# Performance work log

Hardware: AMD Instinct MI355X
Metric: run time of the kernel (lower is better)

The kernel has to match this reference:

```python
import jax, jax.numpy as jnp
import numpy as np

DIM = 1280
HEADS = 16
HEAD_DIM = DIM // HEADS  # 80
N_CHUNKS = 8
CHUNK = 1024
TOTAL = N_CHUNKS * CHUNK  # 8192 packed tokens


def rotate_half(x):
    x1, x2 = jnp.split(x, 2, axis=-1)
    return jnp.concatenate([-x2, x1], axis=-1)


def setup_inputs() -> dict:
    key = jax.random.key(0)
    k0, k1, k2 = jax.random.split(key, 3)
    hidden_states = jax.random.normal(k0, (TOTAL, DIM), dtype=jnp.float32)
    # 2D-rope style per-token angles, duplicated halves (standard vision RoPE layout)
    inv_freq = 1.0 / (10000.0 ** (jnp.arange(0, HEAD_DIM, 2, dtype=jnp.float32) / HEAD_DIM))
    pos = jnp.arange(TOTAL, dtype=jnp.float32)
    freqs = pos[:, None] * inv_freq[None, :]            # [T, HEAD_DIM//2]
    emb = jnp.concatenate([freqs, freqs], axis=-1)      # [T, HEAD_DIM]
    cos = jnp.cos(emb)
    sin = jnp.sin(emb)
    qkv_w = jax.random.normal(k1, (3 * DIM, DIM), dtype=jnp.float32) * 0.02
    qkv_b = jnp.zeros((3 * DIM,), dtype=jnp.float32)
    proj_w = jax.random.normal(k2, (DIM, DIM), dtype=jnp.float32) * 0.02
    proj_b = jnp.zeros((DIM,), dtype=jnp.float32)
    cu_seqlens = (jnp.arange(N_CHUNKS + 1, dtype=jnp.int32) * CHUNK)
    return {"hidden_states": hidden_states, "cos": cos, "sin": sin,
            "qkv_w": qkv_w, "qkv_b": qkv_b, "proj_w": proj_w, "proj_b": proj_b,
            "cu_seqlens": cu_seqlens}


def reference(hidden_states, cos, sin, qkv_w, qkv_b, proj_w, proj_b, cu_seqlens):
    # Equal-length chunks (cu_seqlens uniform): vectorize the Python chunk loop
    # as a leading batch axis n over chunks of length L.
    n = cu_seqlens.shape[0] - 1
    total, dim = hidden_states.shape
    L = total // n
    scaling = HEAD_DIM ** -0.5

    x = hidden_states.reshape(n, L, dim)
    qkv = x @ qkv_w.T + qkv_b                              # [n, L, 3*dim]
    qkv = qkv.reshape(n, L, 3, HEADS, HEAD_DIM)
    q, k, v = qkv[:, :, 0], qkv[:, :, 1], qkv[:, :, 2]     # [n, L, H, hd]

    # inline RoPE in fp32 (matches apply_rotary_pos_emb_vision)
    c = cos.reshape(n, L, 1, HEAD_DIM).astype(jnp.float32)
    s = sin.reshape(n, L, 1, HEAD_DIM).astype(jnp.float32)
    qf = q.astype(jnp.float32)
    kf = k.astype(jnp.float32)
    q = (qf * c + rotate_half(qf) * s).astype(q.dtype)
    k = (kf * c + rotate_half(kf) * s).astype(k.dtype)

    # naive per-chunk full attention: QK^T, fp32 softmax, PV
    scores = jnp.einsum('nlhd,nmhd->nhlm', q, k) * scaling  # [n, H, L, L]
    probs = jax.nn.softmax(scores.astype(jnp.float32), axis=-1).astype(q.dtype)
    out = jnp.einsum('nhlm,nmhd->nlhd', probs, v)           # [n, L, H, hd]
    out = out.reshape(n, L, dim)
    out = out @ proj_w.T + proj_b                           # [n, L, dim]
    return out.reshape(total, dim)
```

## Files before the change

### kernel.cpp

```cpp
#include <hip/hip_runtime.h>
#include <stdint.h>

#define DIM 1280
#define HEADS 16
#define HD 80
#define TOTAL 8192
#define CHUNK 1024
#define QKVN 3840

typedef __attribute__((ext_vector_type(8))) __bf16 bf16x8;
typedef __attribute__((ext_vector_type(4))) float floatx4;

typedef __attribute__((address_space(1))) const uint32_t gu32;
typedef __attribute__((address_space(3))) uint32_t lu32;

__device__ __forceinline__ void llds16(const void* g, void* l) {
  __builtin_amdgcn_global_load_lds((gu32*)g, (lu32*)l, 16, 0, 0);
}

__device__ __forceinline__ unsigned short f2b(float f) {
  union { __bf16 b; unsigned short u; } x; x.b = (__bf16)f; return x.u;
}
__device__ __forceinline__ float b2f(unsigned short u) {
  union { __bf16 b; unsigned short u; } x; x.u = u; return (float)x.b;
}
__device__ __forceinline__ float fexp2(float x) {
#if __has_builtin(__builtin_amdgcn_exp2f)
  return __builtin_amdgcn_exp2f(x);
#else
  return __expf(x * 0.6931471805599453f);
#endif
}

#define QSCALE (0.11180339887498949f * 1.44269504088896340f)

#define QROW 96
#define KT_SH (64 * 104)
#define VT_SH (80 * 72)

__global__ void cvt_bf16(const float* __restrict__ src, unsigned short* __restrict__ dst, int n4) {
  int i = blockIdx.x * 256 + threadIdx.x;
  if (i >= n4) return;
  float4 v = reinterpret_cast<const float4*>(src)[i];
  ushort4 o;
  o.x = f2b(v.x); o.y = f2b(v.y); o.z = f2b(v.z); o.w = f2b(v.w);
  reinterpret_cast<ushort4*>(dst)[i] = o;
}


__device__ __forceinline__ void stage_a64(const unsigned short* __restrict__ G,
                                          unsigned short* ls, int wv, int lane,
                                          int row0, int kk, int hi) {
#pragma unroll
  for (int t = 0; t < 2; ++t) {
    const int stripe = t * 8 + wv;
    const int rb = ((stripe >> 3) << 7) + ((stripe & 7) << 3) + hi;
    const int r = rb + (lane >> 3);
    const int ch = (lane & 7) ^ (r & 7);
    llds16(G + (size_t)(row0 + r) * DIM + kk + (ch << 3), ls + rb * 64);
  }
}

__device__ __forceinline__ void stage_b64(const unsigned short* __restrict__ G,
                                          unsigned short* ls, int wv, int lane,
                                          int row0, int kk, int hi) {
#pragma unroll
  for (int t = 0; t < 2; ++t) {
    const int stripe = t * 8 + wv;
    const int rb = ((stripe >> 2) << 6) + ((stripe & 3) << 3) + hi;
    const int r = rb + (lane >> 3);
    const int ch = (lane & 7) ^ (r & 7);
    llds16(G + (size_t)(row0 + r) * DIM + kk + (ch << 3), ls + rb * 64);
  }
}

__device__ __forceinline__ bf16x8 frg(const unsigned short* ls, int r, int cx) {
  return *reinterpret_cast<const bf16x8*>(ls + r * 64 + (cx << 3));
}

#define MFMA_BF16 __builtin_amdgcn_mfma_f32_16x16x32_bf16
#define LGKM0() asm volatile("s_waitcnt lgkmcnt(0)" ::: "memory")
#define BARR()  asm volatile("s_barrier" ::: "memory")

template<int MODE>
__launch_bounds__(512, 2)
__global__ void gemm8(const unsigned short* __restrict__ A,
                      const unsigned short* __restrict__ B,
                      const float* __restrict__ bias,
                      unsigned short* __restrict__ qo,
                      unsigned short* __restrict__ ko,
                      unsigned short* __restrict__ vo,
                      float* __restrict__ fo) {
  __shared__ __attribute__((aligned(16))) unsigned short lsA[2][256 * 64];
  __shared__ __attribute__((aligned(16))) unsigned short lsB[2][256 * 64];
  const int m0 = blockIdx.x * 256;
  const int n0 = blockIdx.y * 256;
  const int tid = threadIdx.x;
  const int wv = tid >> 6, lane = tid & 63;
  const int wr = wv >> 2, wc = wv & 3;
  const int q4 = lane >> 4, l15 = lane & 15;
  const int sx = l15 & 7;
  const int cx0 = q4 ^ sx;
  const int cx1 = (4 + q4) ^ sx;

  stage_a64(A, &lsA[0][0], wv, lane, m0, 0, 0);
  stage_b64(B, &lsB[0][0], wv, lane, n0, 0, 0);
  stage_b64(B, &lsB[0][0], wv, lane, n0, 0, 32);
  stage_a64(A, &lsA[0][0], wv, lane, m0, 0, 64);
  stage_b64(B, &lsB[1][0], wv, lane, n0, 64, 0);
  stage_a64(A, &lsA[1][0], wv, lane, m0, 64, 0);
  stage_b64(B, &lsB[1][0], wv, lane, n0, 64, 32);

  floatx4 acc[8][4];
#pragma unroll
  for (int i = 0; i < 8; ++i)
#pragma unroll
    for (int j = 0; j < 4; ++j)
      acc[i][j] = (floatx4){0.f, 0.f, 0.f, 0.f};

  asm volatile("s_waitcnt vmcnt(6)" ::: "memory");
  BARR();

  const int rA = wr * 128 + l15;
  const int rB = wc * 64 + l15;

  bf16x8 ArLo[4][2], ArHi[4][2], Blo[2][2], Bhi[2][2];

#pragma unroll 2
  for (int kt = 0; kt < 20; ++kt) {
    const unsigned short* la = &lsA[kt & 1][0];
    const unsigned short* lb = &lsB[kt & 1][0];
    unsigned short* aN = &lsA[(kt & 1) ^ 1][0];
    unsigned short* aC = &lsA[kt & 1][0];
    unsigned short* bC = &lsB[kt & 1][0];
    const bool st1 = (kt + 1 < 20);
    const bool st2 = (kt + 2 < 20);

    if (kt > 0) {
#pragma unroll
      for (int m = 0; m < 4; ++m)
#pragma unroll
        for (int n = 0; n < 2; ++n) {
          acc[m + 4][n] = MFMA_BF16(ArHi[m][0], Blo[n][0], acc[m + 4][n], 0, 0, 0);
          acc[m + 4][n] = MFMA_BF16(ArHi[m][1], Blo[n][1], acc[m + 4][n], 0, 0, 0);
        }
    }
#pragma unroll
    for (int m = 0; m < 4; ++m) {
      ArLo[m][0] = frg(la, rA + m * 16, cx0);
      ArLo[m][1] = frg(la, rA + m * 16, cx1);
    }
#pragma unroll
    for (int n = 0; n < 2; ++n) {
      Blo[n][0] = frg(lb, rB + n * 16, cx0);
      Blo[n][1] = frg(lb, rB + n * 16, cx1);
    }
    if (st1) stage_a64(A, aN, wv, lane, m0, (kt + 1) * 64, 64);
    LGKM0();
    BARR();

#pragma unroll
    for (int m = 0; m < 4; ++m)
#pragma unroll
      for (int n = 0; n < 2; ++n) {
        acc[m][n] = MFMA_BF16(ArLo[m][0], Blo[n][0], acc[m][n], 0, 0, 0);
        acc[m][n] = MFMA_BF16(ArLo[m][1], Blo[n][1], acc[m][n], 0, 0, 0);
      }
#pragma unroll
    for (int n = 0; n < 2; ++n) {
      Bhi[n][0] = frg(lb, rB + (n + 2) * 16, cx0);
      Bhi[n][1] = frg(lb, rB + (n + 2) * 16, cx1);
    }
    if (st2) stage_b64(B, bC, wv, lane, n0, (kt + 2) * 64, 0);
    LGKM0();
    BARR();

#pragma unroll
    for (int m = 0; m < 4; ++m)
#pragma unroll
      for (int n = 0; n < 2; ++n) {
        acc[m][n + 2] = MFMA_BF16(ArLo[m][0], Bhi[n][0], acc[m][n + 2], 0, 0, 0);
        acc[m][n + 2] = MFMA_BF16(ArLo[m][1], Bhi[n][1], acc[m][n + 2], 0, 0, 0);
      }
#pragma unroll
    for (int m = 0; m < 4; ++m) {
      ArHi[m][0] = frg(la, rA + (m + 4) * 16, cx0);
      ArHi[m][1] = frg(la, rA + (m + 4) * 16, cx1);
    }
    if (st2) stage_a64(A, aC, wv, lane, m0, (kt + 2) * 64, 0);
    LGKM0();
    BARR();

#pragma unroll
    for (int m = 0; m < 4; ++m)
#pragma unroll
      for (int n = 0; n < 2; ++n) {
        acc[m + 4][n + 2] = MFMA_BF16(ArHi[m][0], Bhi[n][0], acc[m + 4][n + 2], 0, 0, 0);
        acc[m + 4][n + 2] = MFMA_BF16(ArHi[m][1], Bhi[n][1], acc[m + 4][n + 2], 0, 0, 0);
      }
    if (st2) stage_b64(B, bC, wv, lane, n0, (kt + 2) * 64, 32);
    if (st2)      asm volatile("s_waitcnt vmcnt(6)" ::: "memory");
    else if (st1) asm volatile("s_waitcnt vmcnt(0)" ::: "memory");
    BARR();
  }

#pragma unroll
  for (int m = 0; m < 4; ++m)
#pragma unroll
    for (int n = 0; n < 2; ++n) {
      acc[m + 4][n] = MFMA_BF16(ArHi[m][0], Blo[n][0], acc[m + 4][n], 0, 0, 0);
      acc[m + 4][n] = MFMA_BF16(ArHi[m][1], Blo[n][1], acc[m + 4][n], 0, 0, 0);
    }

  unsigned short* os = nullptr;
  int nloc = n0;
  if (MODE == 0) {
    if (blockIdx.y < 5)       { os = qo; }
    else if (blockIdx.y < 10) { os = ko; nloc = n0 - DIM; }
    else                      { os = vo; nloc = n0 - 2 * DIM; }
  }
#pragma unroll
  for (int n = 0; n < 4; ++n) {
    const int cg = wc * 64 + n * 16 + l15;
    const float bn = bias[n0 + cg];
#pragma unroll
    for (int m = 0; m < 8; ++m) {
#pragma unroll
      for (int r = 0; r < 4; ++r) {
        const int row = m0 + wr * 128 + m * 16 + q4 * 4 + r;
        const float val = acc[m][n][r] + bn;
        if (MODE == 0) os[(size_t)row * DIM + nloc + cg] = f2b(val);
        else           fo[(size_t)row * DIM + n0 + cg] = val;
      }
    }
  }
}

__global__ void prep_q(const unsigned short* __restrict__ qbuf,
                       const float* __restrict__ cp, const float* __restrict__ sp,
                       unsigned short* __restrict__ qimg) {
  const int m = blockIdx.x, tid = threadIdx.x;
  const int ch = m >> 10, rl = m & 1023;
#pragma unroll
  for (int i = 0; i < 3; ++i) {
    const int it = i * 256 + tid;
    if (it < 640) {
      const int h = it / 40, d = it - h * 40;
      const float c = cp[m * HD + d], s = sp[m * HD + d];
      const float x1 = b2f(qbuf[(size_t)m * DIM + h * HD + d]);
      const float x2 = b2f(qbuf[(size_t)m * DIM + h * HD + d + 40]);
      const size_t ob = ((size_t)(ch * 16 + h) * 1024 + rl) * QROW;
      qimg[ob + d]      = f2b((x1 * c - x2 * s) * QSCALE);
      qimg[ob + d + 40] = f2b((x2 * c + x1 * s) * QSCALE);
    }
  }
  { const int h = tid >> 4, c = tid & 15;
    qimg[((size_t)(ch * 16 + h) * 1024 + rl) * QROW + 80 + c] = 0; }
}

__global__ void prep_k(const unsigned short* __restrict__ kbuf,
                       const float* __restrict__ cp, const float* __restrict__ sp,
                       unsigned short* __restrict__ kimg) {
  const int m = blockIdx.x, tid = threadIdx.x;
  const int ch = m >> 10, rl = m & 1023;
  const int jt = rl >> 6, rr = rl & 63;
#pragma unroll
  for (int i = 0; i < 3; ++i) {
    const int it = i * 256 + tid;
    if (it < 640) {
      const int h = it / 40, d = it - h * 40;
      const float c = cp[m * HD + d], s = sp[m * HD + d];
      const float x1 = b2f(kbuf[(size_t)m * DIM + h * HD + d]);
      const float x2 = b2f(kbuf[(size_t)m * DIM + h * HD + d + 40]);
      const size_t ob = ((size_t)((ch * 16 + h) * 16 + jt) * KT_SH) + rr * 104;
      kimg[ob + d]      = f2b(x1 * c - x2 * s);
      kimg[ob + d + 40] = f2b(x2 * c + x1 * s);
    }
  }
#pragma unroll
  for (int i = 0; i < 2; ++i) {
    const int it = i * 256 + tid;
    if (it < 384) {
      const int h = it / 24, c = it - h * 24;
      kimg[((size_t)((ch * 16 + h) * 16 + jt) * KT_SH) + rr * 104 + 80 + c] = 0;
    }
  }
}

__global__ void prep_v(const unsigned short* __restrict__ vbuf,
                       unsigned short* __restrict__ vimg) {
  __shared__ __attribute__((aligned(16))) unsigned short lsT[64 * 88];
  const int bx = blockIdx.x;
  const int jt = bx & 15, h = (bx >> 4) & 15, ch = bx >> 8;
  const int tid = threadIdx.x;
  const int row0 = ch * CHUNK + jt * 64;
#pragma unroll
  for (int i = 0; i < 3; ++i) {
    const int it = i * 256 + tid;
    if (it < 640) {
      const int r = it / 10, c = it - r * 10;
      const uint4 v = *reinterpret_cast<const uint4*>(vbuf + (size_t)(row0 + r) * DIM + h * HD + c * 8);
      *reinterpret_cast<uint4*>(&lsT[r * 88 + c * 8]) = v;
    }
  }
  __syncthreads();
  unsigned short* ot = vimg + (size_t)((ch * 16 + h) * 16 + jt) * VT_SH;
#pragma unroll
  for (int i = 0; i < 12; ++i) {
    const int it = i * 256 + tid;
    if (it < 2880) {
      const int d = it / 36, kk = it - d * 36;
      uint32_t w = 0;
      if (kk < 32) {
        const uint32_t lo = lsT[(2 * kk) * 88 + d];
        const uint32_t hi = lsT[(2 * kk + 1) * 88 + d];
        w = lo | (hi << 16);
      }
      *reinterpret_cast<uint32_t*>(ot + d * 72 + kk * 2) = w;
    }
  }
}

__launch_bounds__(256, 2)
__global__ void attn_k(const unsigned short* __restrict__ qimg,
                       const unsigned short* __restrict__ kimg,
                       const unsigned short* __restrict__ vimg,
                       unsigned short* __restrict__ ob) {
  __shared__ __attribute__((aligned(16))) unsigned short lsK[2][KT_SH];
  __shared__ __attribute__((aligned(16))) unsigned short lsV[2][VT_SH];
  __shared__ __attribute__((aligned(16))) unsigned short lsP[128 * 72];

  const int bx = blockIdx.x;
  const int qt = bx & 7, h = (bx >> 3) & 15, ch = bx >> 7;
  const int tid = threadIdx.x, wv = tid >> 6, lane = tid & 63;
  const int q4 = lane >> 4, l15 = lane & 15;
  const int qrow_loc = qt * 128 + wv * 32;

  bf16x8 aq[2][3];
  {
    const unsigned short* qb = qimg + ((size_t)(ch * 16 + h) * 1024 + qrow_loc) * QROW;
#pragma unroll
    for (int mt = 0; mt < 2; ++mt)
#pragma unroll
      for (int ks = 0; ks < 3; ++ks)
        aq[mt][ks] = *reinterpret_cast<const bf16x8*>(qb + (size_t)(mt * 16 + l15) * QROW + ks * 32 + q4 * 8);
  }

  floatx4 oacc[2][5];
  float lpart[2] = {0.f, 0.f};
#pragma unroll
  for (int mt = 0; mt < 2; ++mt)
#pragma unroll
    for (int t = 0; t < 5; ++t) oacc[mt][t] = (floatx4){0.f, 0.f, 0.f, 0.f};

  const char* kbase = (const char*)(kimg + (size_t)(ch * 16 + h) * 16 * KT_SH);
  const char* vbase = (const char*)(vimg + (size_t)(ch * 16 + h) * 16 * VT_SH);

  auto stage_kv = [&](int jt, char* lk, char* lv) {
    const char* kg = kbase + (size_t)jt * (KT_SH * 2);
#pragma unroll
    for (int r = 0; r < 4; ++r) {
      const int off = (r * 4 + wv) * 1024;
      if (off < KT_SH * 2)
        llds16(kg + off + lane * 16, lk + off);
    }
    const char* vg = vbase + (size_t)jt * (VT_SH * 2);
#pragma unroll
    for (int r = 0; r < 3; ++r) {
      const int off = (r * 4 + wv) * 1024;
      if (off < VT_SH * 2) {
        if (off + 1024 <= VT_SH * 2) llds16(vg + off + lane * 16, lv + off);
        else if (lane < 16)          llds16(vg + off + lane * 16, lv + off);
      }
    }
  };

  stage_kv(0, (char*)lsK[0], (char*)lsV[0]);

  for (int jt = 0; jt < 16; ++jt) {
    const int cur = jt & 1;
    __syncthreads();
    if (jt + 1 < 16)
      stage_kv(jt + 1, (char*)lsK[cur ^ 1], (char*)lsV[cur ^ 1]);

    const unsigned short* lk = lsK[cur];
    const unsigned short* lv = lsV[cur];

    floatx4 sfr[2][4];
    __builtin_amdgcn_s_setprio(1);
#pragma unroll
    for (int c = 0; c < 4; ++c) {
      const bf16x8 ak0 = *reinterpret_cast<const bf16x8*>(&lk[(c * 16 + l15) * 104 + 0  + q4 * 8]);
      const bf16x8 ak1 = *reinterpret_cast<const bf16x8*>(&lk[(c * 16 + l15) * 104 + 32 + q4 * 8]);
      const bf16x8 ak2 = *reinterpret_cast<const bf16x8*>(&lk[(c * 16 + l15) * 104 + 64 + q4 * 8]);
#pragma unroll
      for (int mt = 0; mt < 2; ++mt) {
        floatx4 s = (floatx4){0.f, 0.f, 0.f, 0.f};
        s = __builtin_amdgcn_mfma_f32_16x16x32_bf16(ak0, aq[mt][0], s, 0, 0, 0);
        s = __builtin_amdgcn_mfma_f32_16x16x32_bf16(ak1, aq[mt][1], s, 0, 0, 0);
        s = __builtin_amdgcn_mfma_f32_16x16x32_bf16(ak2, aq[mt][2], s, 0, 0, 0);
        sfr[mt][c] = s;
      }
    }
    __builtin_amdgcn_s_setprio(0);

#pragma unroll
    for (int mt = 0; mt < 2; ++mt)
#pragma unroll
      for (int c = 0; c < 4; ++c) {
        const float p0 = fexp2(sfr[mt][c][0]);
        const float p1 = fexp2(sfr[mt][c][1]);
        const float p2 = fexp2(sfr[mt][c][2]);
        const float p3 = fexp2(sfr[mt][c][3]);
        lpart[mt] += (p0 + p1) + (p2 + p3);
        ushort4 w;
        w.x = f2b(p0); w.y = f2b(p1); w.z = f2b(p2); w.w = f2b(p3);
        *reinterpret_cast<ushort4*>(&lsP[(wv * 32 + mt * 16 + l15) * 72 + c * 16 + q4 * 4]) = w;
      }

    __builtin_amdgcn_s_setprio(1);
#pragma unroll
    for (int ks = 0; ks < 2; ++ks) {
      const bf16x8 ap0 = *reinterpret_cast<const bf16x8*>(&lsP[(wv * 32 + 0  + l15) * 72 + ks * 32 + q4 * 8]);
      const bf16x8 ap1 = *reinterpret_cast<const bf16x8*>(&lsP[(wv * 32 + 16 + l15) * 72 + ks * 32 + q4 * 8]);
#pragma unroll
      for (int t = 0; t < 5; ++t) {
        const bf16x8 bv = *reinterpret_cast<const bf16x8*>(&lv[(t * 16 + l15) * 72 + ks * 32 + q4 * 8]);
        oacc[0][t] = __builtin_amdgcn_mfma_f32_16x16x32_bf16(ap0, bv, oacc[0][t], 0, 0, 0);
        oacc[1][t] = __builtin_amdgcn_mfma_f32_16x16x32_bf16(ap1, bv, oacc[1][t], 0, 0, 0);
      }
    }
    __builtin_amdgcn_s_setprio(0);
  }

#pragma unroll
  for (int mt = 0; mt < 2; ++mt) {
    lpart[mt] += __shfl_xor(lpart[mt], 16, 64);
    lpart[mt] += __shfl_xor(lpart[mt], 32, 64);
  }
  float inv[2];
  inv[0] = 1.0f / lpart[0];
  inv[1] = 1.0f / lpart[1];

  float invr[2][4];
#pragma unroll
  for (int mt = 0; mt < 2; ++mt)
#pragma unroll
    for (int r = 0; r < 4; ++r)
      invr[mt][r] = __shfl(inv[mt], q4 * 4 + r, 64);

#pragma unroll
  for (int mt = 0; mt < 2; ++mt)
#pragma unroll
    for (int t = 0; t < 5; ++t)
#pragma unroll
      for (int r = 0; r < 4; ++r) {
        const int gr = ch * CHUNK + qrow_loc + mt * 16 + q4 * 4 + r;
        const int gc = h * HD + t * 16 + l15;
        ob[(size_t)gr * DIM + gc] = f2b(oacc[mt][t][r] * invr[mt][r]);
      }
}

extern "C" void kernel_launch(void* const* d_in, const int* in_sizes, int n_in,
                              void* d_out, int out_size, void* d_ws, size_t ws_size,
                              hipStream_t stream) {
  (void)in_sizes; (void)n_in; (void)out_size; (void)ws_size;
  const float* hs    = (const float*)d_in[0];
  const float* cosp  = (const float*)d_in[1];
  const float* sinp  = (const float*)d_in[2];
  const float* qkvw  = (const float*)d_in[3];
  const float* qkvb  = (const float*)d_in[4];
  const float* projw = (const float*)d_in[5];
  const float* projb = (const float*)d_in[6];

  char* ws = (char*)d_ws;
  unsigned short* xb   = (unsigned short*)(ws + 0);
  unsigned short* wq   = (unsigned short*)(ws + 20971520);
  unsigned short* qbuf = (unsigned short*)(ws + 30801920);
  unsigned short* kbuf = (unsigned short*)(ws + 51773440);
  unsigned short* vbuf = (unsigned short*)(ws + 72744960);
  unsigned short* wp   = (unsigned short*)(ws + 93716480);
  unsigned short* obuf = (unsigned short*)(ws + 96993280);
  unsigned short* kimg = (unsigned short*)(ws + 117964800);
  unsigned short* qimg = (unsigned short*)(ws + 0);
  unsigned short* vimg = (unsigned short*)(ws + 30801920);

  cvt_bf16<<<TOTAL * DIM / 4 / 256, 256, 0, stream>>>(hs, xb, TOTAL * DIM / 4);
  cvt_bf16<<<QKVN * DIM / 4 / 256, 256, 0, stream>>>(qkvw, wq, QKVN * DIM / 4);
  cvt_bf16<<<DIM * DIM / 4 / 256, 256, 0, stream>>>(projw, wp, DIM * DIM / 4);

  gemm8<0><<<dim3(TOTAL / 256, QKVN / 256), 512, 0, stream>>>(
      xb, wq, qkvb, qbuf, kbuf, vbuf, nullptr);

  prep_q<<<TOTAL, 256, 0, stream>>>(qbuf, cosp, sinp, qimg);
  prep_k<<<TOTAL, 256, 0, stream>>>(kbuf, cosp, sinp, kimg);
  prep_v<<<2048, 256, 0, stream>>>(vbuf, vimg);

  attn_k<<<1024, 256, 0, stream>>>(qimg, kimg, vimg, obuf);

  gemm8<1><<<dim3(TOTAL / 256, DIM / 256), 512, 0, stream>>>(
      obuf, wp, projb, nullptr, nullptr, nullptr, (float*)d_out);
}
```

Baseline: 352.2 us.

## Fuse V transpose into QKV GEMM epilogue and merge vectorized Q/K RoPE prep

The QKV GEMM epilogue now writes V tiles straight into the transposed per-head, per-tile image layout that attention reads. This removes the separate prep_v kernel and the round trip through an intermediate V buffer. The separate prep_q and prep_k kernels are merged into one kernel that applies RoPE with vectorized 4-wide loads and stores, sharing the cos/sin loads between Q and K. Workspace offsets are reshuffled, and the attention output now reuses the qbuf region. The V padding columns are no longer explicitly zeroed, and the V epilogue stores are strided across d rows.

New measurement: 346.2 us. Within noise of the previous version (-1.7%).

```diff
diff --git a/kernel.cpp b/kernel.cpp
--- a/kernel.cpp
+++ b/kernel.cpp
@@ -212,12 +212,48 @@
       acc[m + 4][n] = MFMA_BF16(ArHi[m][1], Blo[n][1], acc[m + 4][n], 0, 0, 0);
     }
 
-  unsigned short* os = nullptr;
-  int nloc = n0;
   if (MODE == 0) {
-    if (blockIdx.y < 5)       { os = qo; }
-    else if (blockIdx.y < 10) { os = ko; nloc = n0 - DIM; }
-    else                      { os = vo; nloc = n0 - 2 * DIM; }
+    if (blockIdx.y >= 10) {
+      const int base_c = n0 - 2 * DIM;
+#pragma unroll
+      for (int n = 0; n < 4; ++n) {
+        const int cg = wc * 64 + n * 16 + l15;
+        const int c = base_c + cg;
+        const int h = c / 80;
+        const int d = c - h * 80;
+        const float bn = bias[2 * DIM + c];
+#pragma unroll
+        for (int m = 0; m < 8; ++m) {
+          const int row = m0 + wr * 128 + m * 16 + q4 * 4;
+          const int chn = row >> 10, jtn = (row >> 6) & 15, krow = row & 63;
+          ushort4 w;
+          w.x = f2b(acc[m][n][0] + bn);
+          w.y = f2b(acc[m][n][1] + bn);
+          w.z = f2b(acc[m][n][2] + bn);
+          w.w = f2b(acc[m][n][3] + bn);
+          *reinterpret_cast<ushort4*>(vo + ((size_t)((chn * 16 + h) * 16 + jtn) * VT_SH) + d * 72 + krow) = w;
+        }
+      }
+      return;
+    }
+    unsigned short* os;
+    int nloc = n0;
+    if (blockIdx.y < 5) { os = qo; }
+    else                { os = ko; nloc = n0 - DIM; }
+#pragma unroll
+    for (int n = 0; n < 4; ++n) {
+      const int cg = wc * 64 + n * 16 + l15;
+      const float bn = bias[n0 + cg];
+#pragma unroll
+      for (int m = 0; m < 8; ++m) {
+#pragma unroll
+        for (int r = 0; r < 4; ++r) {
+          const int row = m0 + wr * 128 + m * 16 + q4 * 4 + r;
+          os[(size_t)row * DIM + nloc + cg] = f2b(acc[m][n][r] + bn);
+        }
+      }
+    }
+    return;
   }
 #pragma unroll
   for (int n = 0; n < 4; ++n) {
@@ -228,96 +264,68 @@
 #pragma unroll
       for (int r = 0; r < 4; ++r) {
         const int row = m0 + wr * 128 + m * 16 + q4 * 4 + r;
-        const float val = acc[m][n][r] + bn;
-        if (MODE == 0) os[(size_t)row * DIM + nloc + cg] = f2b(val);
-        else           fo[(size_t)row * DIM + n0 + cg] = val;
-      }
-    }
-  }
-}
-
-__global__ void prep_q(const unsigned short* __restrict__ qbuf,
-                       const float* __restrict__ cp, const float* __restrict__ sp,
-                       unsigned short* __restrict__ qimg) {
-  const int m = blockIdx.x, tid = threadIdx.x;
-  const int ch = m >> 10, rl = m & 1023;
-#pragma unroll
-  for (int i = 0; i < 3; ++i) {
-    const int it = i * 256 + tid;
-    if (it < 640) {
-      const int h = it / 40, d = it - h * 40;
-      const float c = cp[m * HD + d], s = sp[m * HD + d];
-      const float x1 = b2f(qbuf[(size_t)m * DIM + h * HD + d]);
-      const float x2 = b2f(qbuf[(size_t)m * DIM + h * HD + d + 40]);
-      const size_t ob = ((size_t)(ch * 16 + h) * 1024 + rl) * QROW;
-      qimg[ob + d]      = f2b((x1 * c - x2 * s) * QSCALE);
-      qimg[ob + d + 40] = f2b((x2 * c + x1 * s) * QSCALE);
-    }
-  }
-  { const int h = tid >> 4, c = tid & 15;
-    qimg[((size_t)(ch * 16 + h) * 1024 + rl) * QROW + 80 + c] = 0; }
-}
-
-__global__ void prep_k(const unsigned short* __restrict__ kbuf,
-                       const float* __restrict__ cp, const float* __restrict__ sp,
-                       unsigned short* __restrict__ kimg) {
+        fo[(size_t)row * DIM + n0 + cg] = acc[m][n][r] + bn;
+      }
+    }
+  }
+}
+
+__global__ void prep_qk(const unsigned short* __restrict__ qbuf,
+                        const unsigned short* __restrict__ kbuf,
+                        const float* __restrict__ cp, const float* __restrict__ sp,
+                        unsigned short* __restrict__ qimg,
+                        unsigned short* __restrict__ kimg) {
   const int m = blockIdx.x, tid = threadIdx.x;
   const int ch = m >> 10, rl = m & 1023;
   const int jt = rl >> 6, rr = rl & 63;
-#pragma unroll
-  for (int i = 0; i < 3; ++i) {
-    const int it = i * 256 + tid;
-    if (it < 640) {
-      const int h = it / 40, d = it - h * 40;
-      const float c = cp[m * HD + d], s = sp[m * HD + d];
-      const float x1 = b2f(kbuf[(size_t)m * DIM + h * HD + d]);
-      const float x2 = b2f(kbuf[(size_t)m * DIM + h * HD + d + 40]);
+
+  if (tid < 160) {
+    const int h = tid / 10, j = tid - h * 10;
+    const int d0 = 4 * j;
+    const float4 c4 = *reinterpret_cast<const float4*>(cp + (size_t)m * HD + d0);
+    const float4 s4 = *reinterpret_cast<const float4*>(sp + (size_t)m * HD + d0);
+    {
+      const ushort4 lo = *reinterpret_cast<const ushort4*>(qbuf + (size_t)m * DIM + h * HD + d0);
+      const ushort4 hi = *reinterpret_cast<const ushort4*>(qbuf + (size_t)m * DIM + h * HD + d0 + 40);
+      ushort4 o1, o2;
+      o1.x = f2b((b2f(lo.x) * c4.x - b2f(hi.x) * s4.x) * QSCALE);
+      o1.y = f2b((b2f(lo.y) * c4.y - b2f(hi.y) * s4.y) * QSCALE);
+      o1.z = f2b((b2f(lo.z) * c4.z - b2f(hi.z) * s4.z) * QSCALE);
+      o1.w = f2b((b2f(lo.w) * c4.w - b2f(hi.w) * s4.w) * QSCALE);
+      o2.x = f2b((b2f(hi.x) * c4.x + b2f(lo.x) * s4.x) * QSCALE);
+      o2.y = f2b((b2f(hi.y) * c4.y + b2f(lo.y) * s4.y) * QSCALE);
+      o2.z = f2b((b2f(hi.z) * c4.z + b2f(lo.z) * s4.z) * QSCALE);
+      o2.w = f2b((b2f(hi.w) * c4.w + b2f(lo.w) * s4.w) * QSCALE);
+      const size_t ob = ((size_t)(ch * 16 + h) * 1024 + rl) * QROW;
+      *reinterpret_cast<ushort4*>(qimg + ob + d0) = o1;
+      *reinterpret_cast<ushort4*>(qimg + ob + d0 + 40) = o2;
+    }
+    {
+      const ushort4 lo = *reinterpret_cast<const ushort4*>(kbuf + (size_t)m * DIM + h * HD + d0);
+      const ushort4 hi = *reinterpret_cast<const ushort4*>(kbuf + (size_t)m * DIM + h * HD + d0 + 40);
+      ushort4 o1, o2;
+      o1.x = f2b(b2f(lo.x) * c4.x - b2f(hi.x) * s4.x);
+      o1.y = f2b(b2f(lo.y) * c4.y - b2f(hi.y) * s4.y);
+      o1.z = f2b(b2f(lo.z) * c4.z - b2f(hi.z) * s4.z);
+      o1.w = f2b(b2f(lo.w) * c4.w - b2f(hi.w) * s4.w);
+      o2.x = f2b(b2f(hi.x) * c4.x + b2f(lo.x) * s4.x);
+      o2.y = f2b(b2f(hi.y) * c4.y + b2f(lo.y) * s4.y);
+      o2.z = f2b(b2f(hi.z) * c4.z + b2f(lo.z) * s4.z);
+      o2.w = f2b(b2f(hi.w) * c4.w + b2f(lo.w) * s4.w);
       const size_t ob = ((size_t)((ch * 16 + h) * 16 + jt) * KT_SH) + rr * 104;
-      kimg[ob + d]      = f2b(x1 * c - x2 * s);
-      kimg[ob + d + 40] = f2b(x2 * c + x1 * s);
-    }
-  }
-#pragma unroll
-  for (int i = 0; i < 2; ++i) {
-    const int it = i * 256 + tid;
-    if (it < 384) {
-      const int h = it / 24, c = it - h * 24;
-      kimg[((size_t)((ch * 16 + h) * 16 + jt) * KT_SH) + rr * 104 + 80 + c] = 0;
-    }
-  }
-}
-
-__global__ void prep_v(const unsigned short* __restrict__ vbuf,
-                       unsigned short* __restrict__ vimg) {
-  __shared__ __attribute__((aligned(16))) unsigned short lsT[64 * 88];
-  const int bx = blockIdx.x;
-  const int jt = bx & 15, h = (bx >> 4) & 15, ch = bx >> 8;
-  const int tid = threadIdx.x;
-  const int row0 = ch * CHUNK + jt * 64;
-#pragma unroll
-  for (int i = 0; i < 3; ++i) {
-    const int it = i * 256 + tid;
-    if (it < 640) {
-      const int r = it / 10, c = it - r * 10;
-      const uint4 v = *reinterpret_cast<const uint4*>(vbuf + (size_t)(row0 + r) * DIM + h * HD + c * 8);
-      *reinterpret_cast<uint4*>(&lsT[r * 88 + c * 8]) = v;
-    }
-  }
-  __syncthreads();
-  unsigned short* ot = vimg + (size_t)((ch * 16 + h) * 16 + jt) * VT_SH;
-#pragma unroll
-  for (int i = 0; i < 12; ++i) {
-    const int it = i * 256 + tid;
-    if (it < 2880) {
-      const int d = it / 36, kk = it - d * 36;
-      uint32_t w = 0;
-      if (kk < 32) {
-        const uint32_t lo = lsT[(2 * kk) * 88 + d];
-        const uint32_t hi = lsT[(2 * kk + 1) * 88 + d];
-        w = lo | (hi << 16);
-      }
-      *reinterpret_cast<uint32_t*>(ot + d * 72 + kk * 2) = w;
-    }
+      *reinterpret_cast<ushort4*>(kimg + ob + d0) = o1;
+      *reinterpret_cast<ushort4*>(kimg + ob + d0 + 40) = o2;
+    }
+  }
+  if (tid < 64) {
+    const int h = tid >> 2, qi = tid & 3;
+    const size_t ob = ((size_t)(ch * 16 + h) * 1024 + rl) * QROW;
+    *reinterpret_cast<ushort4*>(qimg + ob + 80 + 4 * qi) = (ushort4){0, 0, 0, 0};
+  } else if (tid < 160) {
+    const int t = tid - 64;
+    const int h = t / 6, qi = t - h * 6;
+    const size_t ob = ((size_t)((ch * 16 + h) * 16 + jt) * KT_SH) + rr * 104;
+    *reinterpret_cast<ushort4*>(kimg + ob + 80 + 4 * qi) = (ushort4){0, 0, 0, 0};
   }
 }
 
@@ -478,23 +486,20 @@
   unsigned short* wq   = (unsigned short*)(ws + 20971520);
   unsigned short* qbuf = (unsigned short*)(ws + 30801920);
   unsigned short* kbuf = (unsigned short*)(ws + 51773440);
-  unsigned short* vbuf = (unsigned short*)(ws + 72744960);
-  unsigned short* wp   = (unsigned short*)(ws + 93716480);
-  unsigned short* obuf = (unsigned short*)(ws + 96993280);
-  unsigned short* kimg = (unsigned short*)(ws + 117964800);
+  unsigned short* vimg = (unsigned short*)(ws + 72744960);
+  unsigned short* wp   = (unsigned short*)(ws + 96337920);
+  unsigned short* kimg = (unsigned short*)(ws + 99614720);
   unsigned short* qimg = (unsigned short*)(ws + 0);
-  unsigned short* vimg = (unsigned short*)(ws + 30801920);
+  unsigned short* obuf = qbuf;
 
   cvt_bf16<<<TOTAL * DIM / 4 / 256, 256, 0, stream>>>(hs, xb, TOTAL * DIM / 4);
   cvt_bf16<<<QKVN * DIM / 4 / 256, 256, 0, stream>>>(qkvw, wq, QKVN * DIM / 4);
   cvt_bf16<<<DIM * DIM / 4 / 256, 256, 0, stream>>>(projw, wp, DIM * DIM / 4);
 
   gemm8<0><<<dim3(TOTAL / 256, QKVN / 256), 512, 0, stream>>>(
-      xb, wq, qkvb, qbuf, kbuf, vbuf, nullptr);
-
-  prep_q<<<TOTAL, 256, 0, stream>>>(qbuf, cosp, sinp, qimg);
-  prep_k<<<TOTAL, 256, 0, stream>>>(kbuf, cosp, sinp, kimg);
-  prep_v<<<2048, 256, 0, stream>>>(vbuf, vimg);
+      xb, wq, qkvb, qbuf, kbuf, vimg, nullptr);
+
+  prep_qk<<<TOTAL, 256, 0, stream>>>(qbuf, kbuf, cosp, sinp, qimg, kimg);
 
   attn_k<<<1024, 256, 0, stream>>>(qimg, kimg, vimg, obuf);
 
```
